# Performance work log

Hardware: AMD Instinct MI355X
Metric: run time of the kernel (lower is better)

The kernel has to match this reference:

```python
import jax, jax.numpy as jnp
import numpy as np

DIM = 1024
N_HEADS = 16
HEAD_DIM = DIM // N_HEADS
SCALE = HEAD_DIM ** 0.5


def setup_inputs() -> dict:
    key = jax.random.key(0)
    k_x, k_wqkv, k_bqkv, k_wp, k_bp = jax.random.split(key, 5)
    B, S = 4, 2048
    x = jax.random.normal(k_x, (B, S, DIM), dtype=jnp.float32)
    # Linear params stored input-major: y = x @ W + b
    std_qkv = 1.0 / np.sqrt(DIM)
    W_qkv = jax.random.uniform(k_wqkv, (DIM, 3 * DIM), jnp.float32, -std_qkv, std_qkv)
    b_qkv = jax.random.uniform(k_bqkv, (3 * DIM,), jnp.float32, -std_qkv, std_qkv)
    W_proj = jax.random.uniform(k_wp, (DIM, DIM), jnp.float32, -std_qkv, std_qkv)
    b_proj = jax.random.uniform(k_bp, (DIM,), jnp.float32, -std_qkv, std_qkv)
    return {"x": x, "W_qkv": W_qkv, "b_qkv": b_qkv, "W_proj": W_proj, "b_proj": b_proj}


def reference(x, W_qkv, b_qkv, W_proj, b_proj):
    B, S, D = x.shape
    qkv = x @ W_qkv + b_qkv                       # [B,S,3D]
    Q, K, V = jnp.split(qkv, 3, axis=-1)          # each [B,S,D]
    def heads(t):                                 # [B,S,D] -> [B,H,S,hd]
        return t.reshape(B, S, N_HEADS, HEAD_DIM).transpose(0, 2, 1, 3)
    Q, K, V = heads(Q), heads(K), heads(V)
    scores = jnp.einsum('bhqd,bhkd->bhqk', Q, K) / SCALE   # [B,H,S,S]
    attn = jax.nn.softmax(scores, axis=-1)
    out = jnp.einsum('bhqk,bhkd->bhqd', attn, V)           # [B,H,S,hd]
    out = out.transpose(0, 2, 1, 3).reshape(B, S, D)
    return out @ W_proj + b_proj
```

## Files before the change

kernel.cpp:

```cpp
#include <hip/hip_runtime.h>
#include <hip/hip_bf16.h>

typedef __attribute__((ext_vector_type(8))) __bf16 bf16x8;
typedef __attribute__((ext_vector_type(4))) float f32x4;
typedef __attribute__((ext_vector_type(16))) float f32x16;
typedef __attribute__((ext_vector_type(4))) unsigned int u32x4;

#define DIM 1024
#define NHEADS 16
#define HDIM 64
#define BATCH 4
#define SEQ 2048
#define ROWS (BATCH * SEQ)
#define SCL 0.18033688011112042f

__device__ inline unsigned short f2bf(float f) {
    __hip_bfloat16 h = __float2bfloat16(f);
    return *reinterpret_cast<unsigned short*>(&h);
}

__device__ inline unsigned int packbf2(float a, float b) {
    unsigned short ua = __builtin_bit_cast(unsigned short, (__bf16)a);
    unsigned short ub = __builtin_bit_cast(unsigned short, (__bf16)b);
    return (unsigned int)ua | ((unsigned int)ub << 16);
}

typedef const __attribute__((address_space(1))) unsigned int* gas_ptr;
typedef __attribute__((address_space(3))) unsigned int* las_ptr;
__device__ inline void gload16(const void* g, void* l) {
    __builtin_amdgcn_global_load_lds((gas_ptr)g, (las_ptr)l, 16, 0, 0);
}

__global__ __launch_bounds__(256) void cast_f32_bf16(const float* __restrict__ in,
                                                     unsigned short* __restrict__ out,
                                                     int n4) {
    int i = blockIdx.x * 256 + threadIdx.x;
    if (i < n4) {
        float4 v = ((const float4*)in)[i];
        ushort4 o;
        o.x = f2bf(v.x); o.y = f2bf(v.y); o.z = f2bf(v.z); o.w = f2bf(v.w);
        ((ushort4*)out)[i] = o;
    }
}

__global__ __launch_bounds__(256) void transpose_cast(const float* __restrict__ in,
                                                      unsigned short* __restrict__ out,
                                                      int R, int C, int srows, float scl) {
    __shared__ float tile[32][33];
    int c0 = blockIdx.x * 32, r0 = blockIdx.y * 32;
    int tx = threadIdx.x & 31, ty = threadIdx.x >> 5;
#pragma unroll
    for (int i = 0; i < 32; i += 8) {
        int r = r0 + ty + i, c = c0 + tx;
        tile[ty + i][tx] = in[(size_t)r * C + c];
    }
    __syncthreads();
#pragma unroll
    for (int i = 0; i < 32; i += 8) {
        int orow = c0 + ty + i, oc = r0 + tx;
        float v = tile[tx][ty + i];
        if (orow < srows) v *= scl;
        out[(size_t)orow * R + oc] = f2bf(v);
    }
}

__global__ __launch_bounds__(256) void gemm_bt_bias(const unsigned short* __restrict__ A,
                                                    const unsigned short* __restrict__ Bt,
                                                    const float* __restrict__ bias,
                                                    unsigned short* __restrict__ Cq,
                                                    unsigned short* __restrict__ Ckv,
                                                    float* __restrict__ Cf,
                                                    int M, int N, int K, int qcols) {
    __shared__ unsigned short As[2][128 * 32];
    __shared__ unsigned short Bs[2][128 * 32];
    const int tid = threadIdx.x;
    const int lane = tid & 63, wave = tid >> 6;
    const int wm = (wave >> 1) * 64, wn = (wave & 1) * 64;
    const int rowA = blockIdx.y * 128, rowB = blockIdx.x * 128;
    const int fr = lane & 15, fo = (lane >> 4) * 8;

    f32x4 acc[4][4] = {};

    for (int k0 = 0; k0 < K; k0 += 64) {
#pragma unroll
        for (int kc = 0; kc < 2; kc++) {
#pragma unroll
            for (int c = 0; c < 2; c++) {
                int o = c * 4096 + tid * 16;
                int r = o >> 6, cb = o & 63;
                int ldsb = c * 4096 + wave * 1024;
                gload16((const char*)A + ((size_t)(rowA + r) * K + k0 + kc * 32) * 2 + cb,
                        (char*)As[kc] + ldsb);
                gload16((const char*)Bt + ((size_t)(rowB + r) * K + k0 + kc * 32) * 2 + cb,
                        (char*)Bs[kc] + ldsb);
            }
        }
        __syncthreads();
#pragma unroll
        for (int kc = 0; kc < 2; kc++) {
            bf16x8 af[4], bfr[4];
#pragma unroll
            for (int i = 0; i < 4; i++) {
                af[i]  = *(const bf16x8*)(As[kc] + (wm + i * 16 + fr) * 32 + fo);
                bfr[i] = *(const bf16x8*)(Bs[kc] + (wn + i * 16 + fr) * 32 + fo);
            }
#pragma unroll
            for (int mi = 0; mi < 4; mi++)
#pragma unroll
                for (int ni = 0; ni < 4; ni++)
                    acc[mi][ni] = __builtin_amdgcn_mfma_f32_16x16x32_bf16(af[mi], bfr[ni],
                                                                          acc[mi][ni], 0, 0, 0);
        }
        __syncthreads();
    }

    const int cn = lane & 15, cm = (lane >> 4) * 4;
    for (int ni = 0; ni < 4; ni++) {
        int gn = rowB + wn + ni * 16 + cn;
        float bv = bias[gn];
        if (gn < qcols) bv *= SCL;
        for (int mi = 0; mi < 4; mi++) {
#pragma unroll
            for (int r = 0; r < 4; r++) {
                int gm = rowA + wm + mi * 16 + cm + r;
                float v = acc[mi][ni][r] + bv;
                if (Cf) Cf[(size_t)gm * N + gn] = v;
                else if (gn < 1024) Cq[(size_t)gm * 1024 + gn] = f2bf(v);
                else Ckv[(size_t)gm * 2048 + (gn - 1024)] = f2bf(v);
            }
        }
    }
}

__global__ __launch_bounds__(256) void pack_kv(const unsigned short* __restrict__ KVb,
                                               unsigned short* __restrict__ Kp,
                                               unsigned short* __restrict__ Vp) {
    __shared__ unsigned short Kt[64][72];
    __shared__ unsigned short Vt[64][68];
    const int tid = threadIdx.x;
    const int gflat = blockIdx.y * gridDim.x + blockIdx.x;
    const int xcd = gflat & 7, slot = gflat >> 3;
    const int by = xcd * 8 + (slot >> 5);
    const int s0 = (slot & 31) * 64;
    const int b = by >> 4, h = by & 15;
    const size_t rowbase = ((size_t)(b * SEQ + s0)) * 2048 + h * 64;
    const int c = (tid & 7) * 8, rr = tid >> 3;
#pragma unroll
    for (int p = 0; p < 2; p++) {
        int row = p * 32 + rr;
        const unsigned short* src = KVb + rowbase + (size_t)row * 2048;
        uint4 kv = *(const uint4*)(src + c);
        uint4 vv = *(const uint4*)(src + 1024 + c);
        *(uint2*)&Kt[row][c]     = make_uint2(kv.x, kv.y);
        *(uint2*)&Kt[row][c + 4] = make_uint2(kv.z, kv.w);
        *(uint2*)&Vt[row][c]     = make_uint2(vv.x, vv.y);
        *(uint2*)&Vt[row][c + 4] = make_uint2(vv.z, vv.w);
    }
    __syncthreads();
#pragma unroll
    for (int half = 0; half < 2; half++) {
        int f = half * 256 + tid;
        int ktl = f >> 8, ks = (f >> 6) & 3, ln = f & 63;
        int mm = ln & 31, hh = ln >> 5;
        uint4 d = *(const uint4*)&Kt[ktl * 32 + mm][ks * 16 + hh * 8];
        *(uint4*)(Kp + (((size_t)by * 64 + (s0 >> 5) + ktl) * 4 + ks) * 512 + ln * 8) = d;
    }
#pragma unroll
    for (int half = 0; half < 2; half++) {
        int f = half * 256 + tid;
        int ksl = f >> 7, dt = (f >> 6) & 1, ln = f & 63;
        int mm = ln & 31, hh = ln >> 5;
        unsigned short tmp[8];
#pragma unroll
        for (int j = 0; j < 8; j++)
            tmp[j] = Vt[ksl * 16 + (j & 3) + 8 * (j >> 2) + 4 * hh][dt * 32 + mm];
        *(uint4*)(Vp + (((size_t)by * 128 + (s0 >> 4) + ksl) * 2 + dt) * 512 + ln * 8) =
            *(uint4*)tmp;
    }
}

__device__ inline void softmax_pv(const f32x16& cfrag, const bf16x8 vf[2][2],
                                  f32x16& o0, f32x16& o1, float& psum) {
    unsigned int pk[8];
    float es[8];
#pragma unroll
    for (int p = 0; p < 8; p++) {
        float e0 = __builtin_amdgcn_exp2f(cfrag[2 * p]);
        float e1 = __builtin_amdgcn_exp2f(cfrag[2 * p + 1]);
        es[p] = e0 + e1;
        pk[p] = packbf2(e0, e1);
    }
    psum += ((es[0] + es[1]) + (es[2] + es[3])) + ((es[4] + es[5]) + (es[6] + es[7]));
    u32x4 lo = {pk[0], pk[1], pk[2], pk[3]};
    u32x4 hi = {pk[4], pk[5], pk[6], pk[7]};
    bf16x8 pa0 = __builtin_bit_cast(bf16x8, lo);
    bf16x8 pa1 = __builtin_bit_cast(bf16x8, hi);
    o0 = __builtin_amdgcn_mfma_f32_32x32x16_bf16(pa0, vf[0][0], o0, 0, 0, 0);
    o1 = __builtin_amdgcn_mfma_f32_32x32x16_bf16(pa0, vf[0][1], o1, 0, 0, 0);
    o0 = __builtin_amdgcn_mfma_f32_32x32x16_bf16(pa1, vf[1][0], o0, 0, 0, 0);
    o1 = __builtin_amdgcn_mfma_f32_32x32x16_bf16(pa1, vf[1][1], o1, 0, 0, 0);
}

__device__ inline void attn_step(const bf16x8 kf[4], const bf16x8 vf[2][2],
                                 const bf16x8 qf[2][4], f32x16 oacc[2][2], float psum[2]) {
    f32x16 cf0 = {}, cf1 = {};
#pragma unroll
    for (int ks = 0; ks < 4; ks++)
        cf0 = __builtin_amdgcn_mfma_f32_32x32x16_bf16(kf[ks], qf[0][ks], cf0, 0, 0, 0);
#pragma unroll
    for (int ks = 0; ks < 4; ks++)
        cf1 = __builtin_amdgcn_mfma_f32_32x32x16_bf16(kf[ks], qf[1][ks], cf1, 0, 0, 0);
    softmax_pv(cf0, vf, oacc[0][0], oacc[0][1], psum[0]);
    softmax_pv(cf1, vf, oacc[1][0], oacc[1][1], psum[1]);
}

__global__ __launch_bounds__(256, 2) void attn_kernel(const unsigned short* __restrict__ Qb,
                                                      const unsigned short* __restrict__ Kp,
                                                      const unsigned short* __restrict__ Vp,
                                                      unsigned short* __restrict__ attnb) {
    __shared__ float Po[2][8 * 256];
    __shared__ float Pl[2][128];
    const int tid = threadIdx.x;
    const int lane = tid & 63, wave = tid >> 6;
    const int qpair = wave >> 1, ksplit = wave & 1;
    const int m31 = lane & 31, h = lane >> 5;
    const int gflat = blockIdx.y * gridDim.x + blockIdx.x;
    const int xcd = gflat & 7, slot = gflat >> 3;
    const int by = xcd * 8 + (slot >> 4);
    const int qb = slot & 15;
    const int b = by >> 4;
    const int bS = b * SEQ, hcol = (by & 15) * HDIM;
    const int q0 = qb * 128 + qpair * 64;

    bf16x8 qf[2][4];
#pragma unroll
    for (int qt = 0; qt < 2; qt++)
#pragma unroll
        for (int ks = 0; ks < 4; ks++)
            qf[qt][ks] = *(const bf16x8*)(Qb + (size_t)(bS + q0 + qt * 32 + m31) * 1024 +
                                          hcol + ks * 16 + h * 8);

    f32x16 oacc[2][2] = {};
    float psum[2] = {0.f, 0.f};

    const unsigned short* kbase = Kp + (size_t)by * 64 * 2048 + lane * 8;
    const unsigned short* vbase = Vp + (size_t)by * 128 * 1024 + lane * 8;

    const int ku0 = ksplit * 32;
    bf16x8 kfa[4], kfb[4];
    {
        const unsigned short* kp = kbase + (size_t)ku0 * 2048;
#pragma unroll
        for (int ks = 0; ks < 4; ks++) kfa[ks] = *(const bf16x8*)(kp + ks * 512);
    }
    for (int ki = 0; ki < 32; ki += 2) {
        {
            int ku = ku0 + ki;
            bf16x8 vf[2][2];
#pragma unroll
            for (int ks = 0; ks < 2; ks++) {
                const unsigned short* vp = vbase + ((size_t)ku * 2 + ks) * 1024;
                vf[ks][0] = *(const bf16x8*)(vp);
                vf[ks][1] = *(const bf16x8*)(vp + 512);
            }
            const unsigned short* kpn = kbase + (size_t)(ku + 1) * 2048;
#pragma unroll
            for (int ks = 0; ks < 4; ks++) kfb[ks] = *(const bf16x8*)(kpn + ks * 512);
            attn_step(kfa, vf, qf, oacc, psum);
        }
        {
            int ku = ku0 + ki + 1;
            bf16x8 vf[2][2];
#pragma unroll
            for (int ks = 0; ks < 2; ks++) {
                const unsigned short* vp = vbase + ((size_t)ku * 2 + ks) * 1024;
                vf[ks][0] = *(const bf16x8*)(vp);
                vf[ks][1] = *(const bf16x8*)(vp + 512);
            }
            int kup = ku0 + ((ki + 2 < 32) ? (ki + 2) : 31);
            const unsigned short* kpn = kbase + (size_t)kup * 2048;
#pragma unroll
            for (int ks = 0; ks < 4; ks++) kfa[ks] = *(const bf16x8*)(kpn + ks * 512);
            attn_step(kfb, vf, qf, oacc, psum);
        }
    }

#pragma unroll
    for (int qt = 0; qt < 2; qt++) {
        if (ksplit == 1) {
#pragma unroll
            for (int dt = 0; dt < 2; dt++)
#pragma unroll
                for (int c = 0; c < 4; c++) {
                    f32x4 v = {oacc[qt][dt][c * 4 + 0], oacc[qt][dt][c * 4 + 1],
                               oacc[qt][dt][c * 4 + 2], oacc[qt][dt][c * 4 + 3]};
                    *(f32x4*)&Po[qpair][(dt * 4 + c) * 256 + lane * 4] = v;
                }
            if (qt == 0)
                *(float2*)&Pl[qpair][lane * 2] = make_float2(psum[0], psum[1]);
        }
        __syncthreads();
        if (ksplit == 0) {
#pragma unroll
            for (int dt = 0; dt < 2; dt++)
#pragma unroll
                for (int c = 0; c < 4; c++) {
                    f32x4 v = *(const f32x4*)&Po[qpair][(dt * 4 + c) * 256 + lane * 4];
#pragma unroll
                    for (int j = 0; j < 4; j++) oacc[qt][dt][c * 4 + j] += v[j];
                }
            if (qt == 0) {
                float2 pl = *(const float2*)&Pl[qpair][lane * 2];
                psum[0] += pl.x; psum[1] += pl.y;
            }
        }
        if (qt == 0) __syncthreads();
    }

    if (ksplit == 0) {
#pragma unroll
        for (int qt = 0; qt < 2; qt++) {
            float lt = psum[qt] + __shfl_xor(psum[qt], 32, 64);
            float rl = 1.f / lt;
#pragma unroll
            for (int r = 0; r < 16; r++) {
                int row = (r & 3) + 8 * (r >> 2) + 4 * h;
                float rlr = __shfl(rl, row, 64);
                size_t orow = (size_t)(bS + q0 + qt * 32 + row) * 1024 + hcol;
                attnb[orow + m31]      = f2bf(oacc[qt][0][r] * rlr);
                attnb[orow + 32 + m31] = f2bf(oacc[qt][1][r] * rlr);
            }
        }
    }
}

extern "C" void kernel_launch(void* const* d_in, const int* in_sizes, int n_in,
                              void* d_out, int out_size, void* d_ws, size_t ws_size,
                              hipStream_t stream) {
    const float* x      = (const float*)d_in[0];
    const float* W_qkv  = (const float*)d_in[1];
    const float* b_qkv  = (const float*)d_in[2];
    const float* W_proj = (const float*)d_in[3];
    const float* b_proj = (const float*)d_in[4];
    float* out = (float*)d_out;

    char* ws = (char*)d_ws;
    unsigned short* x_bf   = (unsigned short*)(ws);
    unsigned short* WqkvT  = (unsigned short*)(ws + 16777216);
    unsigned short* Qb     = (unsigned short*)(ws + 23068672);
    unsigned short* KVb    = (unsigned short*)(ws + 39845888);
    unsigned short* Kp     = (unsigned short*)(ws);
    unsigned short* Vp     = (unsigned short*)(ws + 73400320);
    unsigned short* attnb  = (unsigned short*)(ws + 39845888);
    unsigned short* WprojT = (unsigned short*)(ws + 90177536);

    cast_f32_bf16<<<(ROWS * DIM / 4 + 255) / 256, 256, 0, stream>>>(x, x_bf, ROWS * DIM / 4);
    transpose_cast<<<dim3(3 * DIM / 32, DIM / 32), 256, 0, stream>>>(W_qkv, WqkvT, DIM, 3 * DIM, DIM, SCL);
    transpose_cast<<<dim3(DIM / 32, DIM / 32), 256, 0, stream>>>(W_proj, WprojT, DIM, DIM, 0, 1.f);

    gemm_bt_bias<<<dim3(3 * DIM / 128, ROWS / 128), 256, 0, stream>>>(
        x_bf, WqkvT, b_qkv, Qb, KVb, nullptr, ROWS, 3 * DIM, DIM, DIM);

    pack_kv<<<dim3(SEQ / 64, BATCH * NHEADS), 256, 0, stream>>>(KVb, Kp, Vp);

    attn_kernel<<<dim3(SEQ / 128, BATCH * NHEADS), 256, 0, stream>>>(Qb, Kp, Vp, attnb);

    gemm_bt_bias<<<dim3(DIM / 128, ROWS / 128), 256, 0, stream>>>(
        attnb, WprojT, b_proj, nullptr, nullptr, out, ROWS, DIM, DIM, 0);
}
```

Before: 290.4 us.

## Fuse K/V packing into QKV GEMM epilogue and swizzle blocks across XCDs

The QKV GEMM epilogue now writes K and V tiles directly in the attention kernel's packed layouts. It stages them through per-wave LDS and drops the separate pack_kv kernel, along with the intermediate KVb buffer write and re-read. The GEMM also remaps block indices so consecutive blocks are grouped per XCD, aiming for better L2 locality. Shared memory grows to hold the staging tiles, and the epilogue relies on a waitcnt rather than a barrier for intra-wave LDS ordering.

Result: faster. 271.8 us (-6.4%).

```diff
diff --git a/kernel.cpp b/kernel.cpp
--- a/kernel.cpp
+++ b/kernel.cpp
@@ -68,15 +68,21 @@
                                                     const unsigned short* __restrict__ Bt,
                                                     const float* __restrict__ bias,
                                                     unsigned short* __restrict__ Cq,
-                                                    unsigned short* __restrict__ Ckv,
+                                                    unsigned short* __restrict__ Kp,
+                                                    unsigned short* __restrict__ Vp,
                                                     float* __restrict__ Cf,
                                                     int M, int N, int K, int qcols) {
-    __shared__ unsigned short As[2][128 * 32];
-    __shared__ unsigned short Bs[2][128 * 32];
+    __shared__ unsigned short SMEM[18432];
+    unsigned short* As0 = SMEM;
+    unsigned short* Bs0 = SMEM + 8192;
     const int tid = threadIdx.x;
     const int lane = tid & 63, wave = tid >> 6;
     const int wm = (wave >> 1) * 64, wn = (wave & 1) * 64;
-    const int rowA = blockIdx.y * 128, rowB = blockIdx.x * 128;
+    const int nwg = gridDim.x * gridDim.y;
+    const int gflat = blockIdx.y * gridDim.x + blockIdx.x;
+    const int bidx = (gflat & 7) * (nwg >> 3) + (gflat >> 3);
+    const int bx = bidx % gridDim.x, byy = bidx / gridDim.x;
+    const int rowA = byy * 128, rowB = bx * 128;
     const int fr = lane & 15, fo = (lane >> 4) * 8;
 
     f32x4 acc[4][4] = {};
@@ -90,9 +96,9 @@
                 int r = o >> 6, cb = o & 63;
                 int ldsb = c * 4096 + wave * 1024;
                 gload16((const char*)A + ((size_t)(rowA + r) * K + k0 + kc * 32) * 2 + cb,
-                        (char*)As[kc] + ldsb);
+                        (char*)As0 + kc * 8192 + ldsb);
                 gload16((const char*)Bt + ((size_t)(rowB + r) * K + k0 + kc * 32) * 2 + cb,
-                        (char*)Bs[kc] + ldsb);
+                        (char*)Bs0 + kc * 8192 + ldsb);
             }
         }
         __syncthreads();
@@ -101,8 +107,8 @@
             bf16x8 af[4], bfr[4];
 #pragma unroll
             for (int i = 0; i < 4; i++) {
-                af[i]  = *(const bf16x8*)(As[kc] + (wm + i * 16 + fr) * 32 + fo);
-                bfr[i] = *(const bf16x8*)(Bs[kc] + (wn + i * 16 + fr) * 32 + fo);
+                af[i]  = *(const bf16x8*)(As0 + kc * 4096 + (wm + i * 16 + fr) * 32 + fo);
+                bfr[i] = *(const bf16x8*)(Bs0 + kc * 4096 + (wn + i * 16 + fr) * 32 + fo);
             }
 #pragma unroll
             for (int mi = 0; mi < 4; mi++)
@@ -115,67 +121,72 @@
     }
 
     const int cn = lane & 15, cm = (lane >> 4) * 4;
-    for (int ni = 0; ni < 4; ni++) {
-        int gn = rowB + wn + ni * 16 + cn;
-        float bv = bias[gn];
-        if (gn < qcols) bv *= SCL;
-        for (int mi = 0; mi < 4; mi++) {
-#pragma unroll
-            for (int r = 0; r < 4; r++) {
-                int gm = rowA + wm + mi * 16 + cm + r;
-                float v = acc[mi][ni][r] + bv;
-                if (Cf) Cf[(size_t)gm * N + gn] = v;
-                else if (gn < 1024) Cq[(size_t)gm * 1024 + gn] = f2bf(v);
-                else Ckv[(size_t)gm * 2048 + (gn - 1024)] = f2bf(v);
-            }
-        }
-    }
-}
-
-__global__ __launch_bounds__(256) void pack_kv(const unsigned short* __restrict__ KVb,
-                                               unsigned short* __restrict__ Kp,
-                                               unsigned short* __restrict__ Vp) {
-    __shared__ unsigned short Kt[64][72];
-    __shared__ unsigned short Vt[64][68];
-    const int tid = threadIdx.x;
-    const int gflat = blockIdx.y * gridDim.x + blockIdx.x;
-    const int xcd = gflat & 7, slot = gflat >> 3;
-    const int by = xcd * 8 + (slot >> 5);
-    const int s0 = (slot & 31) * 64;
-    const int b = by >> 4, h = by & 15;
-    const size_t rowbase = ((size_t)(b * SEQ + s0)) * 2048 + h * 64;
-    const int c = (tid & 7) * 8, rr = tid >> 3;
-#pragma unroll
-    for (int p = 0; p < 2; p++) {
-        int row = p * 32 + rr;
-        const unsigned short* src = KVb + rowbase + (size_t)row * 2048;
-        uint4 kv = *(const uint4*)(src + c);
-        uint4 vv = *(const uint4*)(src + 1024 + c);
-        *(uint2*)&Kt[row][c]     = make_uint2(kv.x, kv.y);
-        *(uint2*)&Kt[row][c + 4] = make_uint2(kv.z, kv.w);
-        *(uint2*)&Vt[row][c]     = make_uint2(vv.x, vv.y);
-        *(uint2*)&Vt[row][c + 4] = make_uint2(vv.z, vv.w);
-    }
-    __syncthreads();
-#pragma unroll
-    for (int half = 0; half < 2; half++) {
-        int f = half * 256 + tid;
-        int ktl = f >> 8, ks = (f >> 6) & 3, ln = f & 63;
-        int mm = ln & 31, hh = ln >> 5;
-        uint4 d = *(const uint4*)&Kt[ktl * 32 + mm][ks * 16 + hh * 8];
-        *(uint4*)(Kp + (((size_t)by * 64 + (s0 >> 5) + ktl) * 4 + ks) * 512 + ln * 8) = d;
-    }
-#pragma unroll
-    for (int half = 0; half < 2; half++) {
-        int f = half * 256 + tid;
-        int ksl = f >> 7, dt = (f >> 6) & 1, ln = f & 63;
-        int mm = ln & 31, hh = ln >> 5;
-        unsigned short tmp[8];
-#pragma unroll
-        for (int j = 0; j < 8; j++)
-            tmp[j] = Vt[ksl * 16 + (j & 3) + 8 * (j >> 2) + 4 * hh][dt * 32 + mm];
-        *(uint4*)(Vp + (((size_t)by * 128 + (s0 >> 4) + ksl) * 2 + dt) * 512 + ln * 8) =
-            *(uint4*)tmp;
+    const int gn0 = rowB + wn;
+
+    if (Cf) {
+        for (int ni = 0; ni < 4; ni++) {
+            int gn = gn0 + ni * 16 + cn;
+            float bv = bias[gn];
+            if (gn < qcols) bv *= SCL;
+            for (int mi = 0; mi < 4; mi++) {
+#pragma unroll
+                for (int r = 0; r < 4; r++) {
+                    int gm = rowA + wm + mi * 16 + cm + r;
+                    Cf[(size_t)gm * N + gn] = acc[mi][ni][r] + bv;
+                }
+            }
+        }
+    } else if (gn0 < 1024) {
+        for (int ni = 0; ni < 4; ni++) {
+            int gn = gn0 + ni * 16 + cn;
+            float bv = bias[gn];
+            if (gn < qcols) bv *= SCL;
+            for (int mi = 0; mi < 4; mi++) {
+#pragma unroll
+                for (int r = 0; r < 4; r++) {
+                    int gm = rowA + wm + mi * 16 + cm + r;
+                    Cq[(size_t)gm * 1024 + gn] = f2bf(acc[mi][ni][r] + bv);
+                }
+            }
+        }
+    } else {
+        unsigned short* Lw = SMEM + wave * (64 * 72);
+        for (int ni = 0; ni < 4; ni++) {
+            float bv = bias[gn0 + ni * 16 + cn];
+            for (int mi = 0; mi < 4; mi++) {
+#pragma unroll
+                for (int r = 0; r < 4; r++)
+                    Lw[(mi * 16 + cm + r) * 72 + ni * 16 + cn] = f2bf(acc[mi][ni][r] + bv);
+            }
+        }
+        __builtin_amdgcn_s_waitcnt(0);
+        const int b = rowA >> 11, s0g = rowA & 2047;
+        const int mm = lane & 31, hh = lane >> 5;
+        if (gn0 < 2048) {
+            const int h = (gn0 - 1024) >> 6;
+            const size_t by = (size_t)(b * 16 + h);
+            const int kub = (s0g + wm) >> 5;
+#pragma unroll
+            for (int f = 0; f < 8; f++) {
+                int ktl = f >> 2, ks = f & 3;
+                uint4 d = *(const uint4*)&Lw[(ktl * 32 + mm) * 72 + ks * 16 + hh * 8];
+                *(uint4*)(Kp + ((by * 64 + kub + ktl) * 4 + ks) * 512 + lane * 8) = d;
+            }
+        } else {
+            const int h = (gn0 - 2048) >> 6;
+            const size_t by = (size_t)(b * 16 + h);
+            const int vub = (s0g + wm) >> 4;
+#pragma unroll
+            for (int f = 0; f < 8; f++) {
+                int ksl = f >> 1, dt = f & 1;
+                unsigned short tmp[8];
+#pragma unroll
+                for (int j = 0; j < 8; j++)
+                    tmp[j] = Lw[(ksl * 16 + (j & 3) + 8 * (j >> 2) + 4 * hh) * 72 + dt * 32 + mm];
+                *(uint4*)(Vp + ((by * 128 + vub + ksl) * 2 + dt) * 512 + lane * 8) =
+                    *(uint4*)tmp;
+            }
+        }
     }
 }
 
@@ -348,23 +359,20 @@
     unsigned short* x_bf   = (unsigned short*)(ws);
     unsigned short* WqkvT  = (unsigned short*)(ws + 16777216);
     unsigned short* Qb     = (unsigned short*)(ws + 23068672);
-    unsigned short* KVb    = (unsigned short*)(ws + 39845888);
-    unsigned short* Kp     = (unsigned short*)(ws);
-    unsigned short* Vp     = (unsigned short*)(ws + 73400320);
-    unsigned short* attnb  = (unsigned short*)(ws + 39845888);
-    unsigned short* WprojT = (unsigned short*)(ws + 90177536);
+    unsigned short* Kp     = (unsigned short*)(ws + 39845888);
+    unsigned short* Vp     = (unsigned short*)(ws + 56623104);
+    unsigned short* WprojT = (unsigned short*)(ws + 73400320);
+    unsigned short* attnb  = (unsigned short*)(ws);
 
     cast_f32_bf16<<<(ROWS * DIM / 4 + 255) / 256, 256, 0, stream>>>(x, x_bf, ROWS * DIM / 4);
     transpose_cast<<<dim3(3 * DIM / 32, DIM / 32), 256, 0, stream>>>(W_qkv, WqkvT, DIM, 3 * DIM, DIM, SCL);
     transpose_cast<<<dim3(DIM / 32, DIM / 32), 256, 0, stream>>>(W_proj, WprojT, DIM, DIM, 0, 1.f);
 
     gemm_bt_bias<<<dim3(3 * DIM / 128, ROWS / 128), 256, 0, stream>>>(
-        x_bf, WqkvT, b_qkv, Qb, KVb, nullptr, ROWS, 3 * DIM, DIM, DIM);
-
-    pack_kv<<<dim3(SEQ / 64, BATCH * NHEADS), 256, 0, stream>>>(KVb, Kp, Vp);
+        x_bf, WqkvT, b_qkv, Qb, Kp, Vp, nullptr, ROWS, 3 * DIM, DIM, DIM);
 
     attn_kernel<<<dim3(SEQ / 128, BATCH * NHEADS), 256, 0, stream>>>(Qb, Kp, Vp, attnb);
 
     gemm_bt_bias<<<dim3(DIM / 128, ROWS / 128), 256, 0, stream>>>(
-        attnb, WprojT, b_proj, nullptr, nullptr, out, ROWS, DIM, DIM, 0);
-}
+        attnb, WprojT, b_proj, nullptr, nullptr, nullptr, out, ROWS, DIM, DIM, 0);
+}
```
